# Performance work log

Measured on AMD Instinct MI355X. Metric: run time of the kernel, lower is better.

## Reference

```python
import jax, jax.numpy as jnp
import numpy as np

N = 50000
E = 800000
IN_C = 128
HID = 64
HEADS = 4
NEG_SLOPE = 0.2
EPS = 1e-16


def setup_inputs() -> dict:
    key = jax.random.key(0)
    ks = jax.random.split(key, 12)
    x = jax.random.normal(ks[0], (N, IN_C), dtype=jnp.float32)
    edge_index = jax.random.randint(ks[1], (2, E), 0, N, dtype=jnp.int64)
    # layer 1: in -> (HEADS, HID), concat heads
    W1 = jax.random.normal(ks[2], (IN_C, HEADS * HID), dtype=jnp.float32) * (1.0 / np.sqrt(IN_C))
    a_src1 = jax.random.normal(ks[3], (HEADS, HID), dtype=jnp.float32) * 0.1
    a_dst1 = jax.random.normal(ks[4], (HEADS, HID), dtype=jnp.float32) * 0.1
    b1 = jnp.zeros((HEADS * HID,), dtype=jnp.float32)
    # layer 2: HEADS*HID -> (1, HID)
    W2 = jax.random.normal(ks[5], (HEADS * HID, HID), dtype=jnp.float32) * (1.0 / np.sqrt(HEADS * HID))
    a_src2 = jax.random.normal(ks[6], (1, HID), dtype=jnp.float32) * 0.1
    a_dst2 = jax.random.normal(ks[7], (1, HID), dtype=jnp.float32) * 0.1
    b2 = jnp.zeros((HID,), dtype=jnp.float32)
    return {"x": x, "edge_index": edge_index, "W1": W1, "a_src1": a_src1,
            "a_dst1": a_dst1, "b1": b1, "W2": W2, "a_src2": a_src2,
            "a_dst2": a_dst2, "b2": b2}


def _gat_conv(x, src, dst, W, a_src, a_dst, bias, heads, ch):
    n = x.shape[0]
    h = (x @ W).reshape(n, heads, ch)                       # [N,H,C]
    alpha_s = jnp.einsum('nhc,hc->nh', h, a_src)            # [N,H]
    alpha_d = jnp.einsum('nhc,hc->nh', h, a_dst)            # [N,H]
    e = jax.nn.leaky_relu(alpha_s[src] + alpha_d[dst], NEG_SLOPE)  # [E,H]
    # segment softmax over incoming edges of each dst node
    m = jax.ops.segment_max(e, dst, num_segments=n)         # [N,H]
    ex = jnp.exp(e - m[dst])
    denom = jax.ops.segment_sum(ex, dst, num_segments=n)    # [N,H]
    alpha = ex / (denom[dst] + EPS)                         # [E,H]
    msg = h[src] * alpha[:, :, None]                        # [E,H,C]
    out = jax.ops.segment_sum(msg, dst, num_segments=n)     # [N,H,C]
    return out.reshape(n, heads * ch) + bias


def reference(x, edge_index, W1, a_src1, a_dst1, b1, W2, a_src2, a_dst2, b2):
    src = edge_index[0]
    dst = edge_index[1]
    h = _gat_conv(x, src, dst, W1, a_src1, a_dst1, b1, HEADS, HID)
    h = jax.nn.elu(h)
    h = _gat_conv(h, src, dst, W2, a_src2, a_dst2, b2, 1, HID)
    h = jax.nn.elu(h)
    return h  # [N, HID] (output_dim == hidden_channels so no final linear)
```

## Files before the change

kernel.cpp:

```cpp
#include <hip/hip_runtime.h>
#include <math.h>

#define NN 50000
#define EE 800000
#define IN_C 128
#define HID 64
#define HEADS 4
#define EEP 950000
#define SCAN_BLOCKS ((NN + 255) / 256)
#define EBLOCKS ((EE + 255) / 256)

typedef __attribute__((ext_vector_type(8))) short bf16x8;
typedef __attribute__((ext_vector_type(4))) float f32x4;

#if defined(__has_builtin)
#if __has_builtin(__builtin_amdgcn_fdot2_f32_bf16)
#define HAVE_FDOT2_BF16 1
#endif
#endif


__device__ inline unsigned short f2bf(float f) {
    unsigned u = __float_as_uint(f);
    return (unsigned short)((u + 0x7fff + ((u >> 16) & 1)) >> 16);
}
__device__ inline float bf2f(unsigned short s) {
    return __uint_as_float(((unsigned)s) << 16);
}
__device__ inline unsigned prm(unsigned a, unsigned b, unsigned sel) {
    return __builtin_amdgcn_perm(a, b, sel);
}
#ifdef HAVE_FDOT2_BF16
typedef __attribute__((ext_vector_type(2))) __bf16 bf2v;
__device__ inline float fdot2bf(unsigned h, unsigned w, float acc) {
    return __builtin_amdgcn_fdot2_f32_bf16(__builtin_bit_cast(bf2v, h),
                                           __builtin_bit_cast(bf2v, w), acc, false);
}
#else
__device__ inline float fdot2bf(unsigned h, unsigned w, float acc) {
    return acc + bf2f((unsigned short)(h & 0xffff)) * bf2f((unsigned short)(w & 0xffff))
               + bf2f((unsigned short)(h >> 16)) * bf2f((unsigned short)(w >> 16));
}
#endif

__device__ inline int wave_incl_scan(int v, int lane) {
    #pragma unroll
    for (int off = 1; off < 64; off <<= 1) {
        int t = __shfl_up(v, off);
        if (lane >= off) v += t;
    }
    return v;
}

__device__ inline int block256_excl_scan(int v, int tid, int* ws4) {
    int lane = tid & 63, wv = tid >> 6;
    int incl = wave_incl_scan(v, lane);
    if (lane == 63) ws4[wv] = incl;
    __syncthreads();
    if (tid == 0) {
        int run = 0;
        #pragma unroll
        for (int i = 0; i < 4; i++) { int t = ws4[i]; ws4[i] = run; run += t; }
    }
    __syncthreads();
    return incl + ws4[wv] - v;
}


__global__ void front_kernel(const int* __restrict__ ei, int* __restrict__ deg,
                             unsigned short* __restrict__ rank,
                             const float* __restrict__ W1, unsigned short* __restrict__ W1Thi,
                             unsigned short* __restrict__ W1Tlo,
                             const float* __restrict__ W2, unsigned short* __restrict__ W2Thi,
                             unsigned short* __restrict__ W2Tlo) {
    int b = blockIdx.x;
    int tid = threadIdx.x;
    if (b < EBLOCKS) {
        int i = b * 256 + tid;
        if (i < EE) rank[i] = (unsigned short)atomicAdd(&deg[ei[EE + i]], 1);
    } else if (b < EBLOCKS + 128) {
        int idx = (b - EBLOCKS) * 256 + tid;
        int r = idx >> 8, c = idx & 255;
        float v = W1[idx];
        unsigned short h = f2bf(v);
        W1Thi[c * 128 + r] = h;
        W1Tlo[c * 128 + r] = f2bf(v - bf2f(h));
    } else {
        int idx = (b - EBLOCKS - 128) * 256 + tid;
        int r = idx >> 6, c = idx & 63;
        float v = W2[idx];
        unsigned short h = f2bf(v);
        W2Thi[c * 256 + r] = h;
        W2Tlo[c * 256 + r] = f2bf(v - bf2f(h));
    }
}

__global__ void scan_fill_kernel(const int* __restrict__ deg,
                                 unsigned long long* __restrict__ desc,
                                 int* __restrict__ row_ptr,
                                 unsigned short* __restrict__ csr_src) {
    __shared__ int ws4[4];
    __shared__ int sbase;
    int b = blockIdx.x, tid = threadIdx.x;
    int idx = b * 256 + tid;
    int draw = (idx < NN) ? deg[idx] : 0;
    int d = (draw + 3) & ~3;
    int excl = block256_excl_scan(d, tid, ws4);
    if (tid == 255) {
        unsigned total = (unsigned)(excl + d);
        __threadfence();
        atomicExch(&desc[b], (1ULL << 32) | (unsigned long long)total);
    }
    if (tid < 64) {
        int sum = 0;
        int hi = b;
        while (hi > 0) {
            int lo = hi - 64; if (lo < 0) lo = 0;
            int myi = lo + tid;
            unsigned v = 0;
            if (myi < hi) {
                unsigned long long d8;
                do { d8 = atomicAdd(&desc[myi], 0ULL); } while ((d8 >> 32) == 0);
                v = (unsigned)(d8 & 0xffffffffULL);
            }
            #pragma unroll
            for (int off = 32; off; off >>= 1) v += __shfl_down(v, off);
            v = __shfl(v, 0);
            sum += (int)v;
            hi = lo;
        }
        if (tid == 0) sbase = sum;
    }
    __syncthreads();
    int gbase = sbase;
    if (idx < NN) {
        int rp = gbase + excl;
        row_ptr[idx] = rp;
        for (int p = rp + draw; p < rp + d; ++p) csr_src[p] = 0;
    }
    if (b == gridDim.x - 1 && tid == 255) row_ptr[NN] = gbase + excl + d;
}

__global__ void scatter_kernel(const int* __restrict__ ei, const unsigned short* __restrict__ rank,
                               const int* __restrict__ row_ptr, unsigned short* __restrict__ csr_src) {
    int i = blockIdx.x * blockDim.x + threadIdx.x;
    if (i < EE) {
        int d = ei[EE + i];
        csr_src[row_ptr[d] + (int)rank[i]] = (unsigned short)ei[i];
    }
}

__global__ __launch_bounds__(256) void gemm1_mfma(
        const float* __restrict__ x,
        const unsigned short* __restrict__ Bhi, const unsigned short* __restrict__ Blo,
        const float* __restrict__ a_src, const float* __restrict__ a_dst,
        unsigned short* __restrict__ h1b, float* __restrict__ as1, float* __restrict__ ad1) {
    __shared__ unsigned short Ahi[64][136];
    __shared__ unsigned short Alo[64][136];
    int tid = threadIdx.x;
    int w = tid >> 6, lane = tid & 63;
    int lq = lane >> 4, lr = lane & 15;
    int brow = blockIdx.x * 64;
    {
        int row = tid >> 2;
        int col0 = (tid & 3) * 32;
        int gr = min(brow + row, NN - 1);
        #pragma unroll
        for (int i = 0; i < 32; i += 4) {
            float4 v = *(const float4*)(x + (size_t)gr * 128 + col0 + i);
            unsigned short h0 = f2bf(v.x), h1 = f2bf(v.y), h2 = f2bf(v.z), h3 = f2bf(v.w);
            Ahi[row][col0 + i + 0] = h0; Alo[row][col0 + i + 0] = f2bf(v.x - bf2f(h0));
            Ahi[row][col0 + i + 1] = h1; Alo[row][col0 + i + 1] = f2bf(v.y - bf2f(h1));
            Ahi[row][col0 + i + 2] = h2; Alo[row][col0 + i + 2] = f2bf(v.z - bf2f(h2));
            Ahi[row][col0 + i + 3] = h3; Alo[row][col0 + i + 3] = f2bf(v.w - bf2f(h3));
        }
    }
    __syncthreads();
    f32x4 acc[4][4];
    f32x4 zf = {0.f, 0.f, 0.f, 0.f};
    #pragma unroll
    for (int mi = 0; mi < 4; mi++)
        #pragma unroll
        for (int ni = 0; ni < 4; ni++) acc[mi][ni] = zf;
    #pragma unroll
    for (int q = 0; q < 4; q++) {
        int ko = q * 32 + lq * 8;
        bf16x8 ah[4], al[4];
        #pragma unroll
        for (int mi = 0; mi < 4; mi++) {
            ah[mi] = *(const bf16x8*)(const void*)&Ahi[mi * 16 + lr][ko];
            al[mi] = *(const bf16x8*)(const void*)&Alo[mi * 16 + lr][ko];
        }
        #pragma unroll
        for (int ni = 0; ni < 4; ni++) {
            size_t bo = (size_t)(w * 64 + ni * 16 + lr) * 128 + ko;
            bf16x8 bh = *(const bf16x8*)(const void*)(Bhi + bo);
            bf16x8 bl = *(const bf16x8*)(const void*)(Blo + bo);
            #pragma unroll
            for (int mi = 0; mi < 4; mi++) {
                acc[mi][ni] = __builtin_amdgcn_mfma_f32_16x16x32_bf16(al[mi], bh, acc[mi][ni], 0, 0, 0);
                acc[mi][ni] = __builtin_amdgcn_mfma_f32_16x16x32_bf16(ah[mi], bl, acc[mi][ni], 0, 0, 0);
                acc[mi][ni] = __builtin_amdgcn_mfma_f32_16x16x32_bf16(ah[mi], bh, acc[mi][ni], 0, 0, 0);
            }
        }
    }
    float asv[4], adv[4];
    #pragma unroll
    for (int ni = 0; ni < 4; ni++) {
        asv[ni] = a_src[w * 64 + ni * 16 + lr];
        adv[ni] = a_dst[w * 64 + ni * 16 + lr];
    }
    #pragma unroll
    for (int mi = 0; mi < 4; mi++) {
        f32x4 ps = zf, pd = zf;
        #pragma unroll
        for (int ni = 0; ni < 4; ni++)
            #pragma unroll
            for (int r = 0; r < 4; r++) {
                ps[r] += acc[mi][ni][r] * asv[ni];
                pd[r] += acc[mi][ni][r] * adv[ni];
            }
        #pragma unroll
        for (int m = 1; m < 16; m <<= 1)
            #pragma unroll
            for (int r = 0; r < 4; r++) {
                ps[r] += __shfl_xor(ps[r], m);
                pd[r] += __shfl_xor(pd[r], m);
            }
        #pragma unroll
        for (int r = 0; r < 4; r++) {
            int n = brow + mi * 16 + lq * 4 + r;
            if (lr == 0 && n < NN) { as1[n * 4 + w] = ps[r]; ad1[n * 4 + w] = pd[r]; }
        }
        #pragma unroll
        for (int ni = 0; ni < 4; ni++)
            #pragma unroll
            for (int r = 0; r < 4; r++) {
                int n = brow + mi * 16 + lq * 4 + r;
                if (n < NN)
                    h1b[(size_t)n * 256 + w * 64 + ni * 16 + lr] = f2bf(acc[mi][ni][r]);
            }
    }
}

__global__ __launch_bounds__(256) void gemm2_mfma(
        const unsigned short* __restrict__ Ab,
        const unsigned short* __restrict__ Bhi, const unsigned short* __restrict__ Blo,
        const float* __restrict__ a_src, const float* __restrict__ a_dst,
        unsigned short* __restrict__ g2b, float* __restrict__ as2, float* __restrict__ ad2) {
    int tid = threadIdx.x;
    int w = tid >> 6, lane = tid & 63;
    int lq = lane >> 4, lr = lane & 15;
    int wrow = blockIdx.x * 128 + w * 32;
    f32x4 acc[2][4];
    f32x4 zf = {0.f, 0.f, 0.f, 0.f};
    #pragma unroll
    for (int mi = 0; mi < 2; mi++)
        #pragma unroll
        for (int ni = 0; ni < 4; ni++) acc[mi][ni] = zf;
    int ra = min(wrow + lr, NN - 1);
    int rb = min(wrow + 16 + lr, NN - 1);
    #pragma unroll
    for (int q = 0; q < 8; q++) {
        int ko = q * 32 + lq * 8;
        bf16x8 ah0 = *(const bf16x8*)(const void*)(Ab + (size_t)ra * 256 + ko);
        bf16x8 ah1 = *(const bf16x8*)(const void*)(Ab + (size_t)rb * 256 + ko);
        #pragma unroll
        for (int ni = 0; ni < 4; ni++) {
            size_t bo = (size_t)(ni * 16 + lr) * 256 + ko;
            bf16x8 bh = *(const bf16x8*)(const void*)(Bhi + bo);
            bf16x8 bl = *(const bf16x8*)(const void*)(Blo + bo);
            acc[0][ni] = __builtin_amdgcn_mfma_f32_16x16x32_bf16(ah0, bl, acc[0][ni], 0, 0, 0);
            acc[0][ni] = __builtin_amdgcn_mfma_f32_16x16x32_bf16(ah0, bh, acc[0][ni], 0, 0, 0);
            acc[1][ni] = __builtin_amdgcn_mfma_f32_16x16x32_bf16(ah1, bl, acc[1][ni], 0, 0, 0);
            acc[1][ni] = __builtin_amdgcn_mfma_f32_16x16x32_bf16(ah1, bh, acc[1][ni], 0, 0, 0);
        }
    }
    float asv[4], adv[4];
    #pragma unroll
    for (int ni = 0; ni < 4; ni++) {
        asv[ni] = a_src[ni * 16 + lr];
        adv[ni] = a_dst[ni * 16 + lr];
    }
    #pragma unroll
    for (int mi = 0; mi < 2; mi++) {
        f32x4 ps = zf, pd = zf;
        #pragma unroll
        for (int ni = 0; ni < 4; ni++)
            #pragma unroll
            for (int r = 0; r < 4; r++) {
                ps[r] += acc[mi][ni][r] * asv[ni];
                pd[r] += acc[mi][ni][r] * adv[ni];
            }
        #pragma unroll
        for (int m = 1; m < 16; m <<= 1)
            #pragma unroll
            for (int r = 0; r < 4; r++) {
                ps[r] += __shfl_xor(ps[r], m);
                pd[r] += __shfl_xor(pd[r], m);
            }
        #pragma unroll
        for (int r = 0; r < 4; r++) {
            int n = wrow + mi * 16 + lq * 4 + r;
            if (lr == 0 && n < NN) { as2[n] = ps[r]; ad2[n] = pd[r]; }
        }
        #pragma unroll
        for (int ni = 0; ni < 4; ni++)
            #pragma unroll
            for (int r = 0; r < 4; r++) {
                int n = wrow + mi * 16 + lq * 4 + r;
                if (n < NN)
                    g2b[(size_t)n * 64 + ni * 16 + lr] = f2bf(acc[mi][ni][r]);
            }
    }
}

__global__ __launch_bounds__(256, 4) void agg1_kernel(
        const unsigned short* __restrict__ h1b, const int* __restrict__ row_ptr,
        const int* __restrict__ deg, const unsigned short* __restrict__ csr_src,
        const float* __restrict__ as, const float* __restrict__ ad,
        const float* __restrict__ b1, unsigned short* __restrict__ h2b) {
    __shared__ unsigned ssrc32[4][32];
    __shared__ unsigned wpk[4][4][33];
    int tid = threadIdx.x;
    int wv = tid >> 6, lane = tid & 63;
    int n = blockIdx.x * 4 + wv;
    if (n >= NN) return;
    int start = row_ptr[n], end = row_ptr[n + 1];
    int real_end = start + deg[n];
    int H = lane >> 5, l5 = lane & 31;
    int h = l5 >> 3;
    int hW = lane >> 4;
    int eSub = lane & 15;
    const unsigned short* __restrict__ hp = h1b + l5 * 8;
    float adW = ad[(size_t)n * 4 + hW];
    f32x4 a0 = {0.f, 0.f, 0.f, 0.f}, a1 = {0.f, 0.f, 0.f, 0.f};
    float dsum = 0.f;
    uint4 LA0, LB0, LA1, LB1;
    unsigned wp0, wp1;
    for (int c0 = start; c0 < end; c0 += 64) {
        int m = min(64, end - c0);
        if (lane < (m >> 1))
            ssrc32[wv][lane] = *(const unsigned*)(const void*)(csr_src + c0 + 2 * lane);
        for (int eb = 0; eb < m; eb += 16) {
            int j = eb + eSub;
            unsigned pairw = ssrc32[wv][j >> 1];
            float x = 0.f;
            if (c0 + j < real_end) {
                int s = (int)((pairw >> ((j & 1) << 4)) & 0xffffu);
                float e = as[(size_t)s * 4 + hW] + adW;
                e = fmaxf(e, 0.f) + 0.2f * fminf(e, 0.f);
                x = __expf(e);
                dsum += x;
            }
            unsigned p = f2bf(x);
            unsigned q = (unsigned)__shfl_down((int)p, 1);
            if ((eSub & 1) == 0 && j < m) wpk[wv][hW][j >> 1] = p | (q << 16);
        }
        int G = m >> 2;
        auto LD = [&](int g, uint4& A, uint4& B, unsigned& wp) {
            unsigned both = ssrc32[wv][2 * g + H];
            int ia = (int)(both & 0xffffu), ib = (int)(both >> 16);
            A = *(const uint4*)(const void*)(hp + ia * 256);
            B = *(const uint4*)(const void*)(hp + ib * 256);
            wp = wpk[wv][h][2 * g + H];
        };
        auto CMP = [&](const uint4& A, const uint4& B, unsigned wp) {
            a0.x = fdot2bf(prm(B.x, A.x, 0x05040100), wp, a0.x);
            a0.y = fdot2bf(prm(B.x, A.x, 0x07060302), wp, a0.y);
            a0.z = fdot2bf(prm(B.y, A.y, 0x05040100), wp, a0.z);
            a0.w = fdot2bf(prm(B.y, A.y, 0x07060302), wp, a0.w);
            a1.x = fdot2bf(prm(B.z, A.z, 0x05040100), wp, a1.x);
            a1.y = fdot2bf(prm(B.z, A.z, 0x07060302), wp, a1.y);
            a1.z = fdot2bf(prm(B.w, A.w, 0x05040100), wp, a1.z);
            a1.w = fdot2bf(prm(B.w, A.w, 0x07060302), wp, a1.w);
        };
        LD(0, LA0, LB0, wp0);
        if (G > 1) LD(1, LA1, LB1, wp1);
        int g = 0;
        while (true) {
            CMP(LA0, LB0, wp0);
            if (g + 2 < G) LD(g + 2, LA0, LB0, wp0);
            if (++g >= G) break;
            CMP(LA1, LB1, wp1);
            if (g + 2 < G) LD(g + 2, LA1, LB1, wp1);
            if (++g >= G) break;
        }
    }
    #pragma unroll
    for (int off = 1; off < 16; off <<= 1) dsum += __shfl_xor(dsum, off);
    float den = __shfl(dsum, ((lane & 31) >> 3) << 4);
    a0.x += __shfl_xor(a0.x, 32); a0.y += __shfl_xor(a0.y, 32);
    a0.z += __shfl_xor(a0.z, 32); a0.w += __shfl_xor(a0.w, 32);
    a1.x += __shfl_xor(a1.x, 32); a1.y += __shfl_xor(a1.y, 32);
    a1.z += __shfl_xor(a1.z, 32); a1.w += __shfl_xor(a1.w, 32);
    if (H == 0) {
        float inv = 1.f / (den + 1e-16f);
        float4 bb0 = *(const float4*)(b1 + l5 * 8);
        float4 bb1 = *(const float4*)(b1 + l5 * 8 + 4);
        float r0 = a0.x * inv + bb0.x, r1 = a0.y * inv + bb0.y;
        float r2 = a0.z * inv + bb0.z, r3 = a0.w * inv + bb0.w;
        float r4 = a1.x * inv + bb1.x, r5 = a1.y * inv + bb1.y;
        float r6 = a1.z * inv + bb1.z, r7 = a1.w * inv + bb1.w;
        r0 = r0 > 0.f ? r0 : __expf(r0) - 1.f; r1 = r1 > 0.f ? r1 : __expf(r1) - 1.f;
        r2 = r2 > 0.f ? r2 : __expf(r2) - 1.f; r3 = r3 > 0.f ? r3 : __expf(r3) - 1.f;
        r4 = r4 > 0.f ? r4 : __expf(r4) - 1.f; r5 = r5 > 0.f ? r5 : __expf(r5) - 1.f;
        r6 = r6 > 0.f ? r6 : __expf(r6) - 1.f; r7 = r7 > 0.f ? r7 : __expf(r7) - 1.f;
        uint4 st;
        st.x = (unsigned)f2bf(r0) | ((unsigned)f2bf(r1) << 16);
        st.y = (unsigned)f2bf(r2) | ((unsigned)f2bf(r3) << 16);
        st.z = (unsigned)f2bf(r4) | ((unsigned)f2bf(r5) << 16);
        st.w = (unsigned)f2bf(r6) | ((unsigned)f2bf(r7) << 16);
        *(uint4*)(void*)(h2b + (size_t)n * 256 + l5 * 8) = st;
    }
}

__global__ __launch_bounds__(256, 4) void agg2_kernel(
        const unsigned short* __restrict__ g2b, const int* __restrict__ row_ptr,
        const int* __restrict__ deg, const unsigned short* __restrict__ csr_src,
        const float* __restrict__ as, const float* __restrict__ ad,
        const float* __restrict__ b2, float* __restrict__ out) {
    __shared__ unsigned ssrc32[4][32];
    __shared__ unsigned wpk2[4][32];
    int tid = threadIdx.x;
    int wv = tid >> 6, lane = tid & 63;
    int n = blockIdx.x * 4 + wv;
    if (n >= NN) return;
    int start = row_ptr[n], end = row_ptr[n + 1];
    int real_end = start + deg[n];
    int H = lane >> 5, l5 = lane & 31;
    const unsigned short* __restrict__ gp = g2b + l5 * 2;
    float adv = ad[n];
    float ax = 0.f, ay = 0.f;
    float dsum = 0.f;
    unsigned A0, B0, w0, A1, B1, w1v;
    for (int c0 = start; c0 < end; c0 += 64) {
        int m = min(64, end - c0);
        if (lane < (m >> 1))
            ssrc32[wv][lane] = *(const unsigned*)(const void*)(csr_src + c0 + 2 * lane);
        float x = 0.f;
        if (c0 + lane < real_end) {
            unsigned pw = ssrc32[wv][lane >> 1];
            int s = (int)((pw >> ((lane & 1) << 4)) & 0xffffu);
            float e = as[s] + adv;
            e = fmaxf(e, 0.f) + 0.2f * fminf(e, 0.f);
            x = __expf(e);
            dsum += x;
        }
        unsigned p = f2bf(x);
        unsigned q = (unsigned)__shfl_down((int)p, 1);
        if (((lane & 1) == 0) && lane < m) wpk2[wv][lane >> 1] = p | (q << 16);
        int G = m >> 2;
        auto LD = [&](int g, unsigned& A, unsigned& B, unsigned& wp) {
            unsigned both = ssrc32[wv][2 * g + H];
            int ia = (int)(both & 0xffffu), ib = (int)(both >> 16);
            A = *(const unsigned*)(const void*)(gp + ia * 64);
            B = *(const unsigned*)(const void*)(gp + ib * 64);
            wp = wpk2[wv][2 * g + H];
        };
        auto CMP = [&](unsigned A, unsigned B, unsigned wp) {
            ax = fdot2bf(prm(B, A, 0x05040100), wp, ax);
            ay = fdot2bf(prm(B, A, 0x07060302), wp, ay);
        };
        LD(0, A0, B0, w0);
        if (G > 1) LD(1, A1, B1, w1v);
        int g = 0;
        while (true) {
            CMP(A0, B0, w0);
            if (g + 2 < G) LD(g + 2, A0, B0, w0);
            if (++g >= G) break;
            CMP(A1, B1, w1v);
            if (g + 2 < G) LD(g + 2, A1, B1, w1v);
            if (++g >= G) break;
        }
    }
    #pragma unroll
    for (int off = 32; off; off >>= 1) dsum += __shfl_down(dsum, off);
    dsum = __shfl(dsum, 0);
    ax += __shfl_xor(ax, 32);
    ay += __shfl_xor(ay, 32);
    if (H == 0) {
        float inv = 1.f / (dsum + 1e-16f);
        float2 bv = ((const float2*)b2)[l5];
        float rx = ax * inv + bv.x;
        float ry = ay * inv + bv.y;
        rx = rx > 0.f ? rx : __expf(rx) - 1.f;
        ry = ry > 0.f ? ry : __expf(ry) - 1.f;
        *(float2*)(out + (size_t)n * 64 + l5 * 2) = make_float2(rx, ry);
    }
}


extern "C" void kernel_launch(void* const* d_in, const int* in_sizes, int n_in,
                              void* d_out, int out_size, void* d_ws, size_t ws_size,
                              hipStream_t stream) {
    const float* x      = (const float*)d_in[0];
    const int*   ei     = (const int*)d_in[1];
    const float* W1     = (const float*)d_in[2];
    const float* a_src1 = (const float*)d_in[3];
    const float* a_dst1 = (const float*)d_in[4];
    const float* b1     = (const float*)d_in[5];
    const float* W2     = (const float*)d_in[6];
    const float* a_src2 = (const float*)d_in[7];
    const float* a_dst2 = (const float*)d_in[8];
    const float* b2     = (const float*)d_in[9];
    float* out = (float*)d_out;

    char* base = (char*)d_ws;
    size_t off = 0;
    auto alloc = [&](size_t bytes) -> void* {
        void* p = base + off;
        off = (off + bytes + 255) & ~(size_t)255;
        return p;
    };
    int*   deg     = (int*)alloc(NN * sizeof(int));
    unsigned long long* desc = (unsigned long long*)alloc(SCAN_BLOCKS * sizeof(unsigned long long));
    unsigned short* rank = (unsigned short*)alloc(EE * sizeof(unsigned short));
    int*   row_ptr = (int*)alloc((NN + 1) * sizeof(int));
    unsigned short* csr_src = (unsigned short*)alloc((size_t)EEP * sizeof(unsigned short));
    unsigned short* W1Thi = (unsigned short*)alloc(256 * 128 * 2);
    unsigned short* W1Tlo = (unsigned short*)alloc(256 * 128 * 2);
    unsigned short* W2Thi = (unsigned short*)alloc(64 * 256 * 2);
    unsigned short* W2Tlo = (unsigned short*)alloc(64 * 256 * 2);
    unsigned short* h1b   = (unsigned short*)alloc((size_t)NN * 256 * 2);
    float* as1     = (float*)alloc((size_t)NN * 4 * sizeof(float));
    float* ad1     = (float*)alloc((size_t)NN * 4 * sizeof(float));
    unsigned short* h2b   = (unsigned short*)alloc((size_t)NN * 256 * 2);
    unsigned short* g2b = h1b;
    float* as2 = as1;
    float* ad2 = ad1;

    size_t clear_bytes = (size_t)((char*)(desc + SCAN_BLOCKS) - (char*)deg);
    hipMemsetAsync(deg, 0, clear_bytes, stream);

    front_kernel<<<EBLOCKS + 128 + 64, 256, 0, stream>>>(ei, deg, rank, W1, W1Thi, W1Tlo,
                                                         W2, W2Thi, W2Tlo);
    scan_fill_kernel<<<SCAN_BLOCKS, 256, 0, stream>>>(deg, desc, row_ptr, csr_src);
    scatter_kernel<<<EBLOCKS, 256, 0, stream>>>(ei, rank, row_ptr, csr_src);

    gemm1_mfma<<<(NN + 63) / 64, 256, 0, stream>>>(x, W1Thi, W1Tlo,
                                                   a_src1, a_dst1, h1b, as1, ad1);
    agg1_kernel<<<(NN + 3) / 4, 256, 0, stream>>>(h1b, row_ptr, deg, csr_src,
                                                  as1, ad1, b1, h2b);
    gemm2_mfma<<<(NN + 127) / 128, 256, 0, stream>>>(h2b, W2Thi, W2Tlo,
                                                     a_src2, a_dst2, g2b, as2, ad2);
    agg2_kernel<<<(NN + 3) / 4, 256, 0, stream>>>(g2b, row_ptr, deg, csr_src,
                                                  as2, ad2, b2, out);
}
```

Measured before the change: 285.2 us.

## Slice feature matrices into 32-channel planes and split aggregation by channel slice

Stores the bf16 node features in a sliced layout [slice][node][32] so each 64-byte row slice is contiguous, and rewrites both aggregation kernels so each block handles one 32-channel slice for 16 nodes. Edges are processed 16 at a time, and eight lane groups each gather 8 bytes per source. The aim is a smaller per-slice working set that fits better in L2 during the random-neighbour gathers. The cost is recomputing the attention logits and exponentials once per slice (8x for layer 1), less memory-level parallelism per wave, and no software prefetch pipeline.

After: 386.2 us. 35.4% more time.

```diff
diff --git a/kernel.cpp b/kernel.cpp
--- a/kernel.cpp
+++ b/kernel.cpp
@@ -237,8 +237,10 @@
             #pragma unroll
             for (int r = 0; r < 4; r++) {
                 int n = brow + mi * 16 + lq * 4 + r;
-                if (n < NN)
-                    h1b[(size_t)n * 256 + w * 64 + ni * 16 + lr] = f2bf(acc[mi][ni][r]);
+                if (n < NN) {
+                    int ch = w * 64 + ni * 16 + lr;
+                    h1b[((size_t)(ch >> 5) * NN + n) * 32 + (ch & 31)] = f2bf(acc[mi][ni][r]);
+                }
             }
     }
 }
@@ -263,8 +265,8 @@
     #pragma unroll
     for (int q = 0; q < 8; q++) {
         int ko = q * 32 + lq * 8;
-        bf16x8 ah0 = *(const bf16x8*)(const void*)(Ab + (size_t)ra * 256 + ko);
-        bf16x8 ah1 = *(const bf16x8*)(const void*)(Ab + (size_t)rb * 256 + ko);
+        bf16x8 ah0 = *(const bf16x8*)(const void*)(Ab + ((size_t)q * NN + ra) * 32 + lq * 8);
+        bf16x8 ah1 = *(const bf16x8*)(const void*)(Ab + ((size_t)q * NN + rb) * 32 + lq * 8);
         #pragma unroll
         for (int ni = 0; ni < 4; ni++) {
             size_t bo = (size_t)(ni * 16 + lr) * 256 + ko;
@@ -309,184 +311,160 @@
             #pragma unroll
             for (int r = 0; r < 4; r++) {
                 int n = wrow + mi * 16 + lq * 4 + r;
-                if (n < NN)
-                    g2b[(size_t)n * 64 + ni * 16 + lr] = f2bf(acc[mi][ni][r]);
+                if (n < NN) {
+                    int ch = ni * 16 + lr;
+                    g2b[((size_t)(ch >> 5) * NN + n) * 32 + (ch & 31)] = f2bf(acc[mi][ni][r]);
+                }
             }
     }
 }
 
 __global__ __launch_bounds__(256, 4) void agg1_kernel(
-        const unsigned short* __restrict__ h1b, const int* __restrict__ row_ptr,
-        const int* __restrict__ deg, const unsigned short* __restrict__ csr_src,
+        const unsigned short* __restrict__ h1b,
+        const int* __restrict__ row_ptr, const int* __restrict__ deg,
+        const unsigned short* __restrict__ csr_src,
         const float* __restrict__ as, const float* __restrict__ ad,
         const float* __restrict__ b1, unsigned short* __restrict__ h2b) {
-    __shared__ unsigned ssrc32[4][32];
-    __shared__ unsigned wpk[4][4][33];
+    __shared__ unsigned ssrc32[4][8];
+    __shared__ unsigned wpk[4][8];
     int tid = threadIdx.x;
     int wv = tid >> 6, lane = tid & 63;
-    int n = blockIdx.x * 4 + wv;
-    if (n >= NN) return;
-    int start = row_ptr[n], end = row_ptr[n + 1];
-    int real_end = start + deg[n];
-    int H = lane >> 5, l5 = lane & 31;
-    int h = l5 >> 3;
-    int hW = lane >> 4;
-    int eSub = lane & 15;
-    const unsigned short* __restrict__ hp = h1b + l5 * 8;
-    float adW = ad[(size_t)n * 4 + hW];
-    f32x4 a0 = {0.f, 0.f, 0.f, 0.f}, a1 = {0.f, 0.f, 0.f, 0.f};
-    float dsum = 0.f;
-    uint4 LA0, LB0, LA1, LB1;
-    unsigned wp0, wp1;
-    for (int c0 = start; c0 < end; c0 += 64) {
-        int m = min(64, end - c0);
-        if (lane < (m >> 1))
-            ssrc32[wv][lane] = *(const unsigned*)(const void*)(csr_src + c0 + 2 * lane);
-        for (int eb = 0; eb < m; eb += 16) {
-            int j = eb + eSub;
-            unsigned pairw = ssrc32[wv][j >> 1];
+    int bb = blockIdx.x;
+    int s = bb & 7;
+    int nbase = (bb >> 3) * 16 + wv * 4;
+    int hH = s >> 1;
+    int p = lane >> 3;
+    int c = lane & 7;
+    const unsigned short* __restrict__ hs = h1b + (size_t)s * NN * 32 + c * 4;
+    const float4 bv = *(const float4*)(b1 + s * 32 + c * 4);
+    for (int k = 0; k < 4; ++k) {
+        int n = nbase + k;
+        if (n >= NN) break;
+        int start = row_ptr[n], end = row_ptr[n + 1];
+        int real_end = start + deg[n];
+        float adW = ad[(size_t)n * 4 + hH];
+        f32x4 acc = {0.f, 0.f, 0.f, 0.f};
+        float dsum = 0.f;
+        for (int c0 = start; c0 < end; c0 += 16) {
+            if (lane < 8)
+                ssrc32[wv][lane] = *(const unsigned*)(const void*)(csr_src + c0 + 2 * lane);
             float x = 0.f;
-            if (c0 + j < real_end) {
-                int s = (int)((pairw >> ((j & 1) << 4)) & 0xffffu);
-                float e = as[(size_t)s * 4 + hW] + adW;
+            if (lane < 16 && c0 + lane < real_end) {
+                unsigned pw = ssrc32[wv][lane >> 1];
+                int sid = (int)((pw >> ((lane & 1) << 4)) & 0xffffu);
+                float e = as[(size_t)sid * 4 + hH] + adW;
                 e = fmaxf(e, 0.f) + 0.2f * fminf(e, 0.f);
                 x = __expf(e);
                 dsum += x;
             }
-            unsigned p = f2bf(x);
-            unsigned q = (unsigned)__shfl_down((int)p, 1);
-            if ((eSub & 1) == 0 && j < m) wpk[wv][hW][j >> 1] = p | (q << 16);
-        }
-        int G = m >> 2;
-        auto LD = [&](int g, uint4& A, uint4& B, unsigned& wp) {
-            unsigned both = ssrc32[wv][2 * g + H];
+            unsigned pb = f2bf(x);
+            unsigned qb = (unsigned)__shfl_down((int)pb, 1);
+            if (lane < 16 && (lane & 1) == 0) wpk[wv][lane >> 1] = pb | (qb << 16);
+            unsigned both = ssrc32[wv][p];
             int ia = (int)(both & 0xffffu), ib = (int)(both >> 16);
-            A = *(const uint4*)(const void*)(hp + ia * 256);
-            B = *(const uint4*)(const void*)(hp + ib * 256);
-            wp = wpk[wv][h][2 * g + H];
-        };
-        auto CMP = [&](const uint4& A, const uint4& B, unsigned wp) {
-            a0.x = fdot2bf(prm(B.x, A.x, 0x05040100), wp, a0.x);
-            a0.y = fdot2bf(prm(B.x, A.x, 0x07060302), wp, a0.y);
-            a0.z = fdot2bf(prm(B.y, A.y, 0x05040100), wp, a0.z);
-            a0.w = fdot2bf(prm(B.y, A.y, 0x07060302), wp, a0.w);
-            a1.x = fdot2bf(prm(B.z, A.z, 0x05040100), wp, a1.x);
-            a1.y = fdot2bf(prm(B.z, A.z, 0x07060302), wp, a1.y);
-            a1.z = fdot2bf(prm(B.w, A.w, 0x05040100), wp, a1.z);
-            a1.w = fdot2bf(prm(B.w, A.w, 0x07060302), wp, a1.w);
-        };
-        LD(0, LA0, LB0, wp0);
-        if (G > 1) LD(1, LA1, LB1, wp1);
-        int g = 0;
-        while (true) {
-            CMP(LA0, LB0, wp0);
-            if (g + 2 < G) LD(g + 2, LA0, LB0, wp0);
-            if (++g >= G) break;
-            CMP(LA1, LB1, wp1);
-            if (g + 2 < G) LD(g + 2, LA1, LB1, wp1);
-            if (++g >= G) break;
-        }
-    }
-    #pragma unroll
-    for (int off = 1; off < 16; off <<= 1) dsum += __shfl_xor(dsum, off);
-    float den = __shfl(dsum, ((lane & 31) >> 3) << 4);
-    a0.x += __shfl_xor(a0.x, 32); a0.y += __shfl_xor(a0.y, 32);
-    a0.z += __shfl_xor(a0.z, 32); a0.w += __shfl_xor(a0.w, 32);
-    a1.x += __shfl_xor(a1.x, 32); a1.y += __shfl_xor(a1.y, 32);
-    a1.z += __shfl_xor(a1.z, 32); a1.w += __shfl_xor(a1.w, 32);
-    if (H == 0) {
-        float inv = 1.f / (den + 1e-16f);
-        float4 bb0 = *(const float4*)(b1 + l5 * 8);
-        float4 bb1 = *(const float4*)(b1 + l5 * 8 + 4);
-        float r0 = a0.x * inv + bb0.x, r1 = a0.y * inv + bb0.y;
-        float r2 = a0.z * inv + bb0.z, r3 = a0.w * inv + bb0.w;
-        float r4 = a1.x * inv + bb1.x, r5 = a1.y * inv + bb1.y;
-        float r6 = a1.z * inv + bb1.z, r7 = a1.w * inv + bb1.w;
-        r0 = r0 > 0.f ? r0 : __expf(r0) - 1.f; r1 = r1 > 0.f ? r1 : __expf(r1) - 1.f;
-        r2 = r2 > 0.f ? r2 : __expf(r2) - 1.f; r3 = r3 > 0.f ? r3 : __expf(r3) - 1.f;
-        r4 = r4 > 0.f ? r4 : __expf(r4) - 1.f; r5 = r5 > 0.f ? r5 : __expf(r5) - 1.f;
-        r6 = r6 > 0.f ? r6 : __expf(r6) - 1.f; r7 = r7 > 0.f ? r7 : __expf(r7) - 1.f;
-        uint4 st;
-        st.x = (unsigned)f2bf(r0) | ((unsigned)f2bf(r1) << 16);
-        st.y = (unsigned)f2bf(r2) | ((unsigned)f2bf(r3) << 16);
-        st.z = (unsigned)f2bf(r4) | ((unsigned)f2bf(r5) << 16);
-        st.w = (unsigned)f2bf(r6) | ((unsigned)f2bf(r7) << 16);
-        *(uint4*)(void*)(h2b + (size_t)n * 256 + l5 * 8) = st;
+            uint2 A = *(const uint2*)(const void*)(hs + (size_t)ia * 32);
+            uint2 B = *(const uint2*)(const void*)(hs + (size_t)ib * 32);
+            unsigned wp = wpk[wv][p];
+            acc.x = fdot2bf(prm(B.x, A.x, 0x05040100), wp, acc.x);
+            acc.y = fdot2bf(prm(B.x, A.x, 0x07060302), wp, acc.y);
+            acc.z = fdot2bf(prm(B.y, A.y, 0x05040100), wp, acc.z);
+            acc.w = fdot2bf(prm(B.y, A.y, 0x07060302), wp, acc.w);
+        }
+        dsum += __shfl_xor(dsum, 1);
+        dsum += __shfl_xor(dsum, 2);
+        dsum += __shfl_xor(dsum, 4);
+        dsum += __shfl_xor(dsum, 8);
+        float den = __shfl(dsum, 0);
+        acc.x += __shfl_xor(acc.x, 8); acc.x += __shfl_xor(acc.x, 16); acc.x += __shfl_xor(acc.x, 32);
+        acc.y += __shfl_xor(acc.y, 8); acc.y += __shfl_xor(acc.y, 16); acc.y += __shfl_xor(acc.y, 32);
+        acc.z += __shfl_xor(acc.z, 8); acc.z += __shfl_xor(acc.z, 16); acc.z += __shfl_xor(acc.z, 32);
+        acc.w += __shfl_xor(acc.w, 8); acc.w += __shfl_xor(acc.w, 16); acc.w += __shfl_xor(acc.w, 32);
+        if (lane < 8) {
+            float inv = 1.f / (den + 1e-16f);
+            float r0 = acc.x * inv + bv.x, r1 = acc.y * inv + bv.y;
+            float r2 = acc.z * inv + bv.z, r3 = acc.w * inv + bv.w;
+            r0 = r0 > 0.f ? r0 : __expf(r0) - 1.f;
+            r1 = r1 > 0.f ? r1 : __expf(r1) - 1.f;
+            r2 = r2 > 0.f ? r2 : __expf(r2) - 1.f;
+            r3 = r3 > 0.f ? r3 : __expf(r3) - 1.f;
+            uint2 st;
+            st.x = (unsigned)f2bf(r0) | ((unsigned)f2bf(r1) << 16);
+            st.y = (unsigned)f2bf(r2) | ((unsigned)f2bf(r3) << 16);
+            *(uint2*)(void*)(h2b + ((size_t)s * NN + n) * 32 + c * 4) = st;
+        }
     }
 }
 
 __global__ __launch_bounds__(256, 4) void agg2_kernel(
-        const unsigned short* __restrict__ g2b, const int* __restrict__ row_ptr,
-        const int* __restrict__ deg, const unsigned short* __restrict__ csr_src,
+        const unsigned short* __restrict__ g2b,
+        const int* __restrict__ row_ptr, const int* __restrict__ deg,
+        const unsigned short* __restrict__ csr_src,
         const float* __restrict__ as, const float* __restrict__ ad,
         const float* __restrict__ b2, float* __restrict__ out) {
-    __shared__ unsigned ssrc32[4][32];
-    __shared__ unsigned wpk2[4][32];
+    __shared__ unsigned ssrc32[4][8];
+    __shared__ unsigned wpk[4][8];
     int tid = threadIdx.x;
     int wv = tid >> 6, lane = tid & 63;
-    int n = blockIdx.x * 4 + wv;
-    if (n >= NN) return;
-    int start = row_ptr[n], end = row_ptr[n + 1];
-    int real_end = start + deg[n];
-    int H = lane >> 5, l5 = lane & 31;
-    const unsigned short* __restrict__ gp = g2b + l5 * 2;
-    float adv = ad[n];
-    float ax = 0.f, ay = 0.f;
-    float dsum = 0.f;
-    unsigned A0, B0, w0, A1, B1, w1v;
-    for (int c0 = start; c0 < end; c0 += 64) {
-        int m = min(64, end - c0);
-        if (lane < (m >> 1))
-            ssrc32[wv][lane] = *(const unsigned*)(const void*)(csr_src + c0 + 2 * lane);
-        float x = 0.f;
-        if (c0 + lane < real_end) {
-            unsigned pw = ssrc32[wv][lane >> 1];
-            int s = (int)((pw >> ((lane & 1) << 4)) & 0xffffu);
-            float e = as[s] + adv;
-            e = fmaxf(e, 0.f) + 0.2f * fminf(e, 0.f);
-            x = __expf(e);
-            dsum += x;
-        }
-        unsigned p = f2bf(x);
-        unsigned q = (unsigned)__shfl_down((int)p, 1);
-        if (((lane & 1) == 0) && lane < m) wpk2[wv][lane >> 1] = p | (q << 16);
-        int G = m >> 2;
-        auto LD = [&](int g, unsigned& A, unsigned& B, unsigned& wp) {
-            unsigned both = ssrc32[wv][2 * g + H];
+    int bb = blockIdx.x;
+    int s = bb & 1;
+    int nbase = (bb >> 1) * 16 + wv * 4;
+    int p = lane >> 3;
+    int c = lane & 7;
+    const unsigned short* __restrict__ gs = g2b + (size_t)s * NN * 32 + c * 4;
+    const float4 bv = *(const float4*)(b2 + s * 32 + c * 4);
+    for (int k = 0; k < 4; ++k) {
+        int n = nbase + k;
+        if (n >= NN) break;
+        int start = row_ptr[n], end = row_ptr[n + 1];
+        int real_end = start + deg[n];
+        float adv = ad[n];
+        f32x4 acc = {0.f, 0.f, 0.f, 0.f};
+        float dsum = 0.f;
+        for (int c0 = start; c0 < end; c0 += 16) {
+            if (lane < 8)
+                ssrc32[wv][lane] = *(const unsigned*)(const void*)(csr_src + c0 + 2 * lane);
+            float x = 0.f;
+            if (lane < 16 && c0 + lane < real_end) {
+                unsigned pw = ssrc32[wv][lane >> 1];
+                int sid = (int)((pw >> ((lane & 1) << 4)) & 0xffffu);
+                float e = as[sid] + adv;
+                e = fmaxf(e, 0.f) + 0.2f * fminf(e, 0.f);
+                x = __expf(e);
+                dsum += x;
+            }
+            unsigned pb = f2bf(x);
+            unsigned qb = (unsigned)__shfl_down((int)pb, 1);
+            if (lane < 16 && (lane & 1) == 0) wpk[wv][lane >> 1] = pb | (qb << 16);
+            unsigned both = ssrc32[wv][p];
             int ia = (int)(both & 0xffffu), ib = (int)(both >> 16);
-            A = *(const unsigned*)(const void*)(gp + ia * 64);
-            B = *(const unsigned*)(const void*)(gp + ib * 64);
-            wp = wpk2[wv][2 * g + H];
-        };
-        auto CMP = [&](unsigned A, unsigned B, unsigned wp) {
-            ax = fdot2bf(prm(B, A, 0x05040100), wp, ax);
-            ay = fdot2bf(prm(B, A, 0x07060302), wp, ay);
-        };
-        LD(0, A0, B0, w0);
-        if (G > 1) LD(1, A1, B1, w1v);
-        int g = 0;
-        while (true) {
-            CMP(A0, B0, w0);
-            if (g + 2 < G) LD(g + 2, A0, B0, w0);
-            if (++g >= G) break;
-            CMP(A1, B1, w1v);
-            if (g + 2 < G) LD(g + 2, A1, B1, w1v);
-            if (++g >= G) break;
-        }
-    }
-    #pragma unroll
-    for (int off = 32; off; off >>= 1) dsum += __shfl_down(dsum, off);
-    dsum = __shfl(dsum, 0);
-    ax += __shfl_xor(ax, 32);
-    ay += __shfl_xor(ay, 32);
-    if (H == 0) {
-        float inv = 1.f / (dsum + 1e-16f);
-        float2 bv = ((const float2*)b2)[l5];
-        float rx = ax * inv + bv.x;
-        float ry = ay * inv + bv.y;
-        rx = rx > 0.f ? rx : __expf(rx) - 1.f;
-        ry = ry > 0.f ? ry : __expf(ry) - 1.f;
-        *(float2*)(out + (size_t)n * 64 + l5 * 2) = make_float2(rx, ry);
+            uint2 A = *(const uint2*)(const void*)(gs + (size_t)ia * 32);
+            uint2 B = *(const uint2*)(const void*)(gs + (size_t)ib * 32);
+            unsigned wp = wpk[wv][p];
+            acc.x = fdot2bf(prm(B.x, A.x, 0x05040100), wp, acc.x);
+            acc.y = fdot2bf(prm(B.x, A.x, 0x07060302), wp, acc.y);
+            acc.z = fdot2bf(prm(B.y, A.y, 0x05040100), wp, acc.z);
+            acc.w = fdot2bf(prm(B.y, A.y, 0x07060302), wp, acc.w);
+        }
+        dsum += __shfl_xor(dsum, 1);
+        dsum += __shfl_xor(dsum, 2);
+        dsum += __shfl_xor(dsum, 4);
+        dsum += __shfl_xor(dsum, 8);
+        float den = __shfl(dsum, 0);
+        acc.x += __shfl_xor(acc.x, 8); acc.x += __shfl_xor(acc.x, 16); acc.x += __shfl_xor(acc.x, 32);
+        acc.y += __shfl_xor(acc.y, 8); acc.y += __shfl_xor(acc.y, 16); acc.y += __shfl_xor(acc.y, 32);
+        acc.z += __shfl_xor(acc.z, 8); acc.z += __shfl_xor(acc.z, 16); acc.z += __shfl_xor(acc.z, 32);
+        acc.w += __shfl_xor(acc.w, 8); acc.w += __shfl_xor(acc.w, 16); acc.w += __shfl_xor(acc.w, 32);
+        if (lane < 8) {
+            float inv = 1.f / (den + 1e-16f);
+            float4 r;
+            r.x = acc.x * inv + bv.x; r.y = acc.y * inv + bv.y;
+            r.z = acc.z * inv + bv.z; r.w = acc.w * inv + bv.w;
+            r.x = r.x > 0.f ? r.x : __expf(r.x) - 1.f;
+            r.y = r.y > 0.f ? r.y : __expf(r.y) - 1.f;
+            r.z = r.z > 0.f ? r.z : __expf(r.z) - 1.f;
+            r.w = r.w > 0.f ? r.w : __expf(r.w) - 1.f;
+            *(float4*)(out + (size_t)n * 64 + s * 32 + c * 4) = r;
+        }
     }
 }
 
@@ -540,10 +518,11 @@
 
     gemm1_mfma<<<(NN + 63) / 64, 256, 0, stream>>>(x, W1Thi, W1Tlo,
                                                    a_src1, a_dst1, h1b, as1, ad1);
-    agg1_kernel<<<(NN + 3) / 4, 256, 0, stream>>>(h1b, row_ptr, deg, csr_src,
-                                                  as1, ad1, b1, h2b);
+    int nblk = (NN + 15) / 16;
+    agg1_kernel<<<nblk * 8, 256, 0, stream>>>(h1b, row_ptr, deg, csr_src,
+                                              as1, ad1, b1, h2b);
     gemm2_mfma<<<(NN + 127) / 128, 256, 0, stream>>>(h2b, W2Thi, W2Tlo,
                                                      a_src2, a_dst2, g2b, as2, ad2);
-    agg2_kernel<<<(NN + 3) / 4, 256, 0, stream>>>(g2b, row_ptr, deg, csr_src,
-                                                  as2, ad2, b2, out);
-}
+    agg2_kernel<<<nblk * 2, 256, 0, stream>>>(g2b, row_ptr, deg, csr_src,
+                                              as2, ad2, b2, out);
+}
```
